# Kernel optimization log

Measured on AMD Instinct MI355X. Metric: run time of the kernel, lower is better.

Reference implementation:

```python
import jax, jax.numpy as jnp
import numpy as np
import math

D_MODEL = 1024
N_HEAD = 16          # sub-heads per branch
N_BR = 4             # hardcoded n_branches
DH = D_MODEL // N_HEAD
H_TOT = N_BR * N_HEAD
B, T = 1, 1024
SCALE = math.pi / math.sqrt(3.0)
ATTNSCALE = DH ** -0.5


def _rope(x):
    # x: [B, H, T, D]; matches torch RoPE: even/odd split, concat halves
    t_len, d = x.shape[2], x.shape[-1]
    inv_freq = 1.0 / (10000.0 ** (jnp.arange(0, d, 2, dtype=jnp.float32) / d))
    freqs = jnp.arange(t_len, dtype=jnp.float32)[:, None] * inv_freq[None, :]  # [T, D/2]
    cos, sin = jnp.cos(freqs), jnp.sin(freqs)
    x1, x2 = x[..., 0::2], x[..., 1::2]
    return jnp.concatenate([-x2 * sin + x1 * cos, x1 * sin + x2 * cos], axis=-1)


def setup_inputs() -> dict:
    key = jax.random.key(0)
    ks = jax.random.split(key, 12)
    s = D_MODEL ** -0.5
    return {
        "X": jax.random.normal(ks[0], (B, T, D_MODEL), jnp.float32),
        "W_Q": jax.random.normal(ks[1], (D_MODEL, D_MODEL * N_BR), jnp.float32) * s,
        "b_Q": jax.random.normal(ks[2], (D_MODEL * N_BR,), jnp.float32) * 0.02,
        "W_K": jax.random.normal(ks[3], (D_MODEL, D_MODEL), jnp.float32) * s,
        "b_K": jax.random.normal(ks[4], (D_MODEL,), jnp.float32) * 0.02,
        "W_V": jax.random.normal(ks[5], (D_MODEL, D_MODEL), jnp.float32) * s,
        "b_V": jax.random.normal(ks[6], (D_MODEL,), jnp.float32) * 0.02,
        "sink_scalars": jax.random.uniform(ks[7], (H_TOT,), jnp.float32, 0.0, 0.1),
        "v_nulls": jax.random.normal(ks[8], (N_BR, D_MODEL), jnp.float32) * 0.02,
        "W_O": jax.random.normal(ks[9], (N_BR, D_MODEL, D_MODEL), jnp.float32) * s,
        "W_O_bias": jax.random.normal(ks[10], (N_BR, D_MODEL), jnp.float32) * 0.02,
    }


def reference(X, W_Q, b_Q, W_K, b_K, W_V, b_V, sink_scalars, v_nulls, W_O, W_O_bias):
    Bv, Tv, C = X.shape
    # projections -> [B, H, T, Dh]
    q = (X @ W_Q + b_Q).reshape(Bv, Tv, H_TOT, DH).transpose(0, 2, 1, 3)
    k_base = (X @ W_K + b_K).reshape(Bv, Tv, N_HEAD, DH).transpose(0, 2, 1, 3)
    v_base = (X @ W_V + b_V).reshape(Bv, Tv, N_HEAD, DH).transpose(0, 2, 1, 3)
    k = jnp.tile(k_base, (1, N_BR, 1, 1))
    v = jnp.tile(v_base, (1, N_BR, 1, 1))
    q, k = _rope(q), _rope(k)

    scores = jnp.einsum("bhtd,bhsd->bhts", q, k) * ATTNSCALE
    key_self = jnp.clip(jnp.sum(k * k, axis=-1), 1e-6, None)      # [B,H,S]
    w = jax.nn.softplus(scores / jnp.sqrt(key_self)[:, :, None, :])
    causal = jnp.tril(jnp.ones((Tv, Tv), bool))                    # [T,S]
    w = jnp.where(causal, w, 0.0)
    w = w * jax.nn.sigmoid(SCALE * w)
    sinks = sink_scalars.reshape(1, H_TOT, 1, 1)
    w = jnp.where(w < sinks, 0.0, w)
    # concat-with-sink renormalization, expressed without the concat
    total = jnp.sum(w, axis=-1, keepdims=True) + sinks + 1e-6      # [B,H,T,1]
    probs_tokens = w / total
    probs_sink = sinks / total                                     # [B,H,T,1]

    out = jnp.einsum("bhts,bhsd->bhtd", probs_tokens, v)
    v_null = v_nulls.reshape(H_TOT, DH)[None, :, None, :]          # [1,H,1,Dh]
    out = out + probs_sink * v_null

    context = out.reshape(Bv, N_BR, N_HEAD, Tv, DH).transpose(0, 1, 3, 2, 4)
    context = context.reshape(Bv, N_BR, Tv, C)
    y = jnp.einsum("bntc,ncd->bntd", context, W_O) + W_O_bias[None, :, None, :]
    return y.mean(axis=1)
```

## Files before the change

### kernel.cpp

```cpp
#include <hip/hip_runtime.h>
#include <math.h>

typedef __attribute__((ext_vector_type(4))) float  f32x4;
typedef __attribute__((ext_vector_type(8))) short  bf16x8;
typedef __attribute__((ext_vector_type(4))) short  s16x4;

#define D_MODEL 1024
#define T_LEN   1024
#define H_TOT   64
#define N_HEAD  16
#define DH      64
#define SQUISH_SCALE 1.8137993642342178f

__device__ __forceinline__ float b2f(short u) {
    union { float f; unsigned b; } v; v.b = ((unsigned)(unsigned short)u) << 16; return v.f;
}
__device__ __forceinline__ short f2b(float f) {
    union { float f; unsigned b; } v; v.f = f;
    unsigned r = (v.b + 0x7FFFu + ((v.b >> 16) & 1u)) >> 16;
    return (short)r;
}
__device__ __forceinline__ unsigned cvt_pk_bf16(float lo, float hi) {
    unsigned r;
    asm("v_cvt_pk_bf16_f32 %0, %1, %2" : "=v"(r) : "v"(lo), "v"(hi));
    return r;
}
__device__ __forceinline__ void gll16(const void* g, void* l) {
    __builtin_amdgcn_global_load_lds((const __attribute__((address_space(1))) void*)g,
                                     (__attribute__((address_space(3))) void*)l, 16, 0, 0);
}

__global__ void convert_x_kernel(const float* __restrict__ src, short* __restrict__ dst) {
    int i = (blockIdx.x * 256 + threadIdx.x) * 4;
    f32x4 v = *(const f32x4*)(src + i);
    s16x4 o;
    o.x = f2b(v.x); o.y = f2b(v.y); o.z = f2b(v.z); o.w = f2b(v.w);
    *(s16x4*)(dst + i) = o;
}

__global__ __launch_bounds__(256) void transpose_convert_kernel(
    const float* __restrict__ src, int R, int C, short* __restrict__ dst, float scale) {
    __shared__ float tile[64][65];
    int c0 = blockIdx.x * 64, r0 = blockIdx.y * 64;
    int tid = threadIdx.x;
    #pragma unroll
    for (int it = 0; it < 16; ++it) {
        int lin = it * 256 + tid;
        int r = lin >> 6, c = lin & 63;
        tile[r][c] = src[(size_t)(r0 + r) * C + c0 + c];
    }
    __syncthreads();
    #pragma unroll
    for (int it = 0; it < 16; ++it) {
        int lin = it * 256 + tid;
        int cc = lin >> 6, rr = lin & 63;
        dst[(size_t)(c0 + cc) * R + r0 + rr] = f2b(tile[rr][cc] * scale);
    }
}

__global__ void bias_setup_kernel(const float* __restrict__ bQ, const float* __restrict__ bK,
                                  const float* __restrict__ bV, const float* __restrict__ bO,
                                  float* __restrict__ biasQKV, float* __restrict__ bias_mean) {
    int i = blockIdx.x * 256 + threadIdx.x;
    if (i < 4096)      biasQKV[i] = bQ[i];
    else if (i < 5120) biasQKV[i] = bK[i - 4096];
    else if (i < 6144) biasQKV[i] = bV[i - 5120];
    else if (i < 7168) {
        int c = i - 6144;
        bias_mean[c] = 0.25f * (bO[c] + bO[1024 + c] + bO[2048 + c] + bO[3072 + c]);
    }
}

__global__ void init_out_kernel(const float* __restrict__ bias_mean, float* __restrict__ out) {
    int i = (blockIdx.x * 256 + threadIdx.x) * 4;
    f32x4 v;
    v.x = bias_mean[(i)     & 1023];
    v.y = bias_mean[(i + 1) & 1023];
    v.z = bias_mean[(i + 2) & 1023];
    v.w = bias_mean[(i + 3) & 1023];
    *(f32x4*)(out + i) = v;
}

__global__ __launch_bounds__(256) void gemm_bt_kernel(
    const short* __restrict__ A, const short* __restrict__ BT,
    const float* __restrict__ bias, short* __restrict__ outB,
    int M, int N, int K) {
    __shared__ short lA[128][64];
    __shared__ short lB[128][64];
    const int tid = threadIdx.x;
    const int lane = tid & 63, wave = tid >> 6;
    const int l15 = lane & 15, l4 = lane >> 4;
    const int wr = wave >> 1, wc = wave & 1;
    const int n0 = blockIdx.x * 128, m0 = blockIdx.y * 128;

    f32x4 acc[4][4];
    const f32x4 fz = {0.f, 0.f, 0.f, 0.f};
    #pragma unroll
    for (int m = 0; m < 4; ++m)
        #pragma unroll
        for (int n = 0; n < 4; ++n) acc[m][n] = fz;

    for (int k0 = 0; k0 < K; k0 += 64) {
        __syncthreads();
        #pragma unroll
        for (int it = 0; it < 4; ++it) {
            int lin0 = it * 256 + wave * 64;
            int lin = lin0 + lane;
            int r = lin >> 3, c = (lin & 7) ^ (r & 7);
            gll16(A  + (size_t)(m0 + r) * K + k0 + c * 8, (char*)lA + lin0 * 16);
            gll16(BT + (size_t)(n0 + r) * K + k0 + c * 8, (char*)lB + lin0 * 16);
        }
        __syncthreads();
        #pragma unroll
        for (int kk = 0; kk < 2; ++kk) {
            bf16x8 af[4], bf_[4];
            #pragma unroll
            for (int m = 0; m < 4; ++m) {
                int row = wr * 64 + m * 16 + l15;
                int ch = (kk * 4 + l4) ^ (row & 7);
                af[m] = *(const bf16x8*)&lA[row][ch << 3];
            }
            #pragma unroll
            for (int n = 0; n < 4; ++n) {
                int row = wc * 64 + n * 16 + l15;
                int ch = (kk * 4 + l4) ^ (row & 7);
                bf_[n] = *(const bf16x8*)&lB[row][ch << 3];
            }
            #pragma unroll
            for (int m = 0; m < 4; ++m)
                #pragma unroll
                for (int n = 0; n < 4; ++n)
                    acc[m][n] = __builtin_amdgcn_mfma_f32_16x16x32_bf16(af[m], bf_[n], acc[m][n], 0, 0, 0);
        }
    }
    #pragma unroll
    for (int m = 0; m < 4; ++m)
        #pragma unroll
        for (int n = 0; n < 4; ++n)
            #pragma unroll
            for (int r = 0; r < 4; ++r) {
                int row = m0 + wr * 64 + m * 16 + l4 * 4 + r;
                int col = n0 + wc * 64 + n * 16 + l15;
                outB[(size_t)row * N + col] = f2b(acc[m][n][r] + bias[col]);
            }
}

__global__ __launch_bounds__(256) void gemm_bt64_splitk_kernel(
    const short* __restrict__ A, const short* __restrict__ BT,
    float* __restrict__ out, int M, int N, int K, int KSLICE) {
    __shared__ short lA[64][64];
    __shared__ short lB[64][64];
    const int tid = threadIdx.x;
    const int lane = tid & 63, wave = tid >> 6;
    const int l15 = lane & 15, l4 = lane >> 4;
    const int wr = wave >> 1, wc = wave & 1;
    const int n0 = blockIdx.x * 64, m0 = blockIdx.y * 64;
    const int kbeg = blockIdx.z * KSLICE, kend = kbeg + KSLICE;

    f32x4 acc[2][2];
    const f32x4 fz = {0.f, 0.f, 0.f, 0.f};
    #pragma unroll
    for (int m = 0; m < 2; ++m)
        #pragma unroll
        for (int n = 0; n < 2; ++n) acc[m][n] = fz;

    for (int k0 = kbeg; k0 < kend; k0 += 64) {
        __syncthreads();
        #pragma unroll
        for (int it = 0; it < 2; ++it) {
            int lin0 = it * 256 + wave * 64;
            int lin = lin0 + lane;
            int r = lin >> 3, c = (lin & 7) ^ (r & 7);
            gll16(A  + (size_t)(m0 + r) * K + k0 + c * 8, (char*)lA + lin0 * 16);
            gll16(BT + (size_t)(n0 + r) * K + k0 + c * 8, (char*)lB + lin0 * 16);
        }
        __syncthreads();
        #pragma unroll
        for (int kk = 0; kk < 2; ++kk) {
            bf16x8 af[2], bf_[2];
            #pragma unroll
            for (int m = 0; m < 2; ++m) {
                int row = wr * 32 + m * 16 + l15;
                int ch = (kk * 4 + l4) ^ (row & 7);
                af[m] = *(const bf16x8*)&lA[row][ch << 3];
            }
            #pragma unroll
            for (int n = 0; n < 2; ++n) {
                int row = wc * 32 + n * 16 + l15;
                int ch = (kk * 4 + l4) ^ (row & 7);
                bf_[n] = *(const bf16x8*)&lB[row][ch << 3];
            }
            #pragma unroll
            for (int m = 0; m < 2; ++m)
                #pragma unroll
                for (int n = 0; n < 2; ++n)
                    acc[m][n] = __builtin_amdgcn_mfma_f32_16x16x32_bf16(af[m], bf_[n], acc[m][n], 0, 0, 0);
        }
    }
    #pragma unroll
    for (int m = 0; m < 2; ++m)
        #pragma unroll
        for (int n = 0; n < 2; ++n)
            #pragma unroll
            for (int r = 0; r < 4; ++r) {
                int row = m0 + wr * 32 + m * 16 + l4 * 4 + r;
                int col = n0 + wc * 32 + n * 16 + l15;
                unsafeAtomicAdd(&out[(size_t)row * N + col], acc[m][n][r]);
            }
}

__global__ __launch_bounds__(128) void rope_qk_kernel(short* __restrict__ QKVb, float* __restrict__ ksr) {
    int t = blockIdx.x;
    int hl = threadIdx.x >> 5;
    int j  = threadIdx.x & 31;
    int head = blockIdx.y * 4 + hl;
    short* p;
    if (head < 64) p = QKVb + (size_t)t * 6144 + head * 64;
    else           p = QKVb + (size_t)t * 6144 + 4096 + (head - 64) * 64;
    float x1 = b2f(p[2 * j]), x2 = b2f(p[2 * j + 1]);
    float freq = (float)t * __builtin_exp2f(-(float)j * 0.41524101186092033f);
    float sn = __sinf(freq), cs = __cosf(freq);
    float o1 = x1 * cs - x2 * sn;
    float o2 = x1 * sn + x2 * cs;
    p[j]      = f2b(o1);
    p[32 + j] = f2b(o2);
    if (head >= 64) {
        float ss = o1 * o1 + o2 * o2;
        #pragma unroll
        for (int off = 16; off; off >>= 1) ss += __shfl_xor(ss, off, 32);
        if (j == 0) ksr[(head - 64) * 1024 + t] = 0.125f * rsqrtf(fmaxf(ss, 1e-6f));
    }
}

__global__ __launch_bounds__(256) void v_transpose_kernel(const short* __restrict__ QKVb, short* __restrict__ Vtb) {
    __shared__ short tile[64][72];
    int h = blockIdx.x, t0 = blockIdx.y * 64;
    int tid = threadIdx.x;
    #pragma unroll
    for (int it = 0; it < 16; ++it) {
        int lin = it * 256 + tid;
        int r = lin >> 6, d = lin & 63;
        tile[r][d] = QKVb[(size_t)(t0 + r) * 6144 + 5120 + h * 64 + d];
    }
    __syncthreads();
    #pragma unroll
    for (int it = 0; it < 16; ++it) {
        int lin = it * 256 + tid;
        int d = lin >> 6, c = lin & 63;
        Vtb[(size_t)(h * 64 + d) * 1024 + t0 + c] = tile[c][d];
    }
}

__global__ __launch_bounds__(256, 4) void attn_kernel(
    const short* __restrict__ QKVb, const short* __restrict__ Vtb,
    const float* __restrict__ ksr, const float* __restrict__ sinks,
    const float* __restrict__ vnulls, short* __restrict__ Ob) {
    __shared__ short lK[64][64];
    __shared__ short lV[64][64];
    __shared__ float lks[64];
    __shared__ float lvn[64];
    __shared__ short lP[4][16][64];

    const int tid = threadIdx.x;
    const int lane = tid & 63, wave = tid >> 6;
    const int l15 = lane & 15, l4 = lane >> 4;
    const int h = blockIdx.x;
    const int qt = 15 - blockIdx.y;
    const int h16 = h & 15;
    const int t0 = qt * 64;
    const float sink = sinks[h];
    if (tid < 64) lvn[tid] = vnulls[h * 64 + tid];

    const int q_abs = t0 + wave * 16 + l15;
    bf16x8 aq[2];
    #pragma unroll
    for (int kk = 0; kk < 2; ++kk)
        aq[kk] = *(const bf16x8*)(QKVb + (size_t)q_abs * 6144 + h * 64 + kk * 32 + l4 * 8);

    const f32x4 fz = {0.f, 0.f, 0.f, 0.f};
    f32x4 acc_o[4];
    #pragma unroll
    for (int n = 0; n < 4; ++n) acc_o[n] = fz;
    float tot = 0.f;

    const int nkt = qt + 1;
    for (int kt = 0; kt < nkt; ++kt) {
        int s0 = kt * 64;
        __syncthreads();
        #pragma unroll
        for (int it = 0; it < 2; ++it) {
            int lin0 = it * 256 + wave * 64;
            int lin = lin0 + lane;
            int r = lin >> 3, c = (lin & 7) ^ (r & 7);
            gll16(QKVb + (size_t)(s0 + r) * 6144 + 4096 + h16 * 64 + c * 8, (char*)lK + lin0 * 16);
            gll16(Vtb + (size_t)(h16 * 64 + r) * 1024 + s0 + c * 8,          (char*)lV + lin0 * 16);
        }
        if (tid < 64) lks[tid] = ksr[h16 * 1024 + s0 + tid];
        __syncthreads();

        f32x4 accs[4];
        #pragma unroll
        for (int n = 0; n < 4; ++n) accs[n] = fz;
        #pragma unroll
        for (int kk = 0; kk < 2; ++kk) {
            bf16x8 bk[4];
            #pragma unroll
            for (int n = 0; n < 4; ++n) {
                int row = n * 16 + l15;
                int ch = (kk * 4 + l4) ^ (row & 7);
                bk[n] = *(const bf16x8*)&lK[row][ch << 3];
            }
            #pragma unroll
            for (int n = 0; n < 4; ++n)
                accs[n] = __builtin_amdgcn_mfma_f32_16x16x32_bf16(bk[n], aq[kk], accs[n], 0, 0, 0);
        }

        #pragma unroll
        for (int n = 0; n < 4; ++n) {
            f32x4 ksv = *(const f32x4*)&lks[n * 16 + l4 * 4];
            float w4[4];
            #pragma unroll
            for (int r = 0; r < 4; ++r) {
                int k_abs = s0 + n * 16 + l4 * 4 + r;
                float z = accs[n][r] * ksv[r];
                float e = __expf(-fabsf(z));
                float w = fmaxf(z, 0.f) + __logf(1.f + e);
                w = (k_abs <= q_abs) ? w : 0.f;
                float g = __expf(-SQUISH_SCALE * w);
                w = w * __builtin_amdgcn_rcpf(1.f + g);
                w = (w >= sink) ? w : 0.f;
                tot += w;
                w4[r] = w;
            }
            unsigned pa = cvt_pk_bf16(w4[0], w4[1]);
            unsigned pb = cvt_pk_bf16(w4[2], w4[3]);
            int ch = (2 * n + (l4 >> 1)) ^ (l15 & 7);
            uint2 val; val.x = pa; val.y = pb;
            *(uint2*)&lP[wave][l15][ch * 8 + (l4 & 1) * 4] = val;
        }

        #pragma unroll
        for (int kk = 0; kk < 2; ++kk) {
            bf16x8 ap = *(const bf16x8*)&lP[wave][l15][((kk * 4 + l4) ^ (l15 & 7)) << 3];
            bf16x8 bv[4];
            #pragma unroll
            for (int n = 0; n < 4; ++n) {
                int row = n * 16 + l15;
                int ch = (kk * 4 + l4) ^ (row & 7);
                bv[n] = *(const bf16x8*)&lV[row][ch << 3];
            }
            #pragma unroll
            for (int n = 0; n < 4; ++n)
                acc_o[n] = __builtin_amdgcn_mfma_f32_16x16x32_bf16(ap, bv[n], acc_o[n], 0, 0, 0);
        }
    }

    tot += __shfl_xor(tot, 16, 64);
    tot += __shfl_xor(tot, 32, 64);
    float tq[4];
    #pragma unroll
    for (int r = 0; r < 4; ++r) tq[r] = __shfl(tot, l4 * 4 + r, 64);

    #pragma unroll
    for (int r = 0; r < 4; ++r) {
        float inv = __builtin_amdgcn_rcpf(tq[r] + sink + 1e-6f);
        int trow = t0 + wave * 16 + l4 * 4 + r;
        #pragma unroll
        for (int n = 0; n < 4; ++n) {
            int d = n * 16 + l15;
            float val = (acc_o[n][r] + sink * lvn[d]) * inv;
            Ob[(size_t)trow * 4096 + h * 64 + d] = f2b(val);
        }
    }
}

extern "C" void kernel_launch(void* const* d_in, const int* in_sizes, int n_in,
                              void* d_out, int out_size, void* d_ws, size_t ws_size,
                              hipStream_t stream) {
    const float* X        = (const float*)d_in[0];
    const float* W_Q      = (const float*)d_in[1];
    const float* b_Q      = (const float*)d_in[2];
    const float* W_K      = (const float*)d_in[3];
    const float* b_K      = (const float*)d_in[4];
    const float* W_V      = (const float*)d_in[5];
    const float* b_V      = (const float*)d_in[6];
    const float* sinks    = (const float*)d_in[7];
    const float* v_nulls  = (const float*)d_in[8];
    const float* W_O      = (const float*)d_in[9];
    const float* W_O_bias = (const float*)d_in[10];
    float* out = (float*)d_out;
    char* ws = (char*)d_ws;

    short* Xb        = (short*)(ws + 0);
    short* WbT       = (short*)(ws + 2097152);
    short* WoT       = (short*)(ws + 14680064);
    short* QKVb      = (short*)(ws + 23068672);
    short* Vtb       = (short*)(ws + 35651584);
    short* Ob        = (short*)(ws + 37748736);
    float* ksr       = (float*)(ws + 46137344);
    float* biasQKV   = (float*)(ws + 46202880);
    float* bias_mean = (float*)(ws + 46227456);

    convert_x_kernel<<<1024, 256, 0, stream>>>(X, Xb);
    transpose_convert_kernel<<<dim3(64, 16), 256, 0, stream>>>(W_Q, 1024, 4096, WbT, 1.f);
    transpose_convert_kernel<<<dim3(16, 16), 256, 0, stream>>>(W_K, 1024, 1024, WbT + 4096 * 1024, 1.f);
    transpose_convert_kernel<<<dim3(16, 16), 256, 0, stream>>>(W_V, 1024, 1024, WbT + 5120 * 1024, 1.f);
    transpose_convert_kernel<<<dim3(16, 64), 256, 0, stream>>>(W_O, 4096, 1024, WoT, 0.25f);
    bias_setup_kernel<<<28, 256, 0, stream>>>(b_Q, b_K, b_V, W_O_bias, biasQKV, bias_mean);

    gemm_bt_kernel<<<dim3(48, 8), 256, 0, stream>>>(Xb, WbT, biasQKV, QKVb, 1024, 6144, 1024);
    rope_qk_kernel<<<dim3(1024, 20), 128, 0, stream>>>(QKVb, ksr);
    v_transpose_kernel<<<dim3(16, 16), 256, 0, stream>>>(QKVb, Vtb);
    attn_kernel<<<dim3(64, 16), 256, 0, stream>>>(QKVb, Vtb, ksr, sinks, v_nulls, Ob);

    init_out_kernel<<<1024, 256, 0, stream>>>(bias_mean, out);
    gemm_bt64_splitk_kernel<<<dim3(16, 16, 4), 256, 0, stream>>>(Ob, WoT, out, 1024, 1024, 4096, 1024);
}
```

Measured before the change: 217.4 us.

## Fuse prep kernels, double-buffer GEMM and attention loads, retile split-K

Merges the X conversion, the weight transpose-converts, the bias setup and the output init into one prep kernel with vectorized loads and stores. It also merges RoPE and the V transpose into one launch. Both GEMMs and the attention kernel now double-buffer their LDS tiles, issuing the next tile's global-to-LDS loads before computing the current one, with explicit waitcnt and barriers. The output-projection split-K GEMM moves to 128x128 tiles with 8 K-slices, and attention occupancy drops to 3 blocks per SM. The goal is fewer launches and hidden load latency, paid for with more LDS use and lower occupancy.

After: 207.9 us. 1.05x faster.

```diff
diff --git a/kernel.cpp b/kernel.cpp
--- a/kernel.cpp
+++ b/kernel.cpp
@@ -5,11 +5,6 @@
 typedef __attribute__((ext_vector_type(8))) short  bf16x8;
 typedef __attribute__((ext_vector_type(4))) short  s16x4;
 
-#define D_MODEL 1024
-#define T_LEN   1024
-#define H_TOT   64
-#define N_HEAD  16
-#define DH      64
 #define SQUISH_SCALE 1.8137993642342178f
 
 __device__ __forceinline__ float b2f(short u) {
@@ -29,64 +24,87 @@
     __builtin_amdgcn_global_load_lds((const __attribute__((address_space(1))) void*)g,
                                      (__attribute__((address_space(3))) void*)l, 16, 0, 0);
 }
-
-__global__ void convert_x_kernel(const float* __restrict__ src, short* __restrict__ dst) {
-    int i = (blockIdx.x * 256 + threadIdx.x) * 4;
-    f32x4 v = *(const f32x4*)(src + i);
-    s16x4 o;
-    o.x = f2b(v.x); o.y = f2b(v.y); o.z = f2b(v.z); o.w = f2b(v.w);
-    *(s16x4*)(dst + i) = o;
-}
-
-__global__ __launch_bounds__(256) void transpose_convert_kernel(
-    const float* __restrict__ src, int R, int C, short* __restrict__ dst, float scale) {
+__device__ __forceinline__ void gll4(const void* g, void* l) {
+    __builtin_amdgcn_global_load_lds((const __attribute__((address_space(1))) void*)g,
+                                     (__attribute__((address_space(3))) void*)l, 4, 0, 0);
+}
+
+__device__ __forceinline__ void do_transpose(const float* __restrict__ src, int R, int C,
+                                             short* __restrict__ dst, float scale,
+                                             int c0, int r0, float (*tile)[65], int tid) {
+    #pragma unroll
+    for (int it = 0; it < 4; ++it) {
+        int lin = it * 256 + tid;
+        int r = lin >> 4, c4 = lin & 15;
+        f32x4 v = *(const f32x4*)(src + (size_t)(r0 + r) * C + c0 + c4 * 4);
+        #pragma unroll
+        for (int k = 0; k < 4; ++k) tile[r][c4 * 4 + k] = v[k];
+    }
+    __syncthreads();
+    #pragma unroll
+    for (int it = 0; it < 4; ++it) {
+        int lin = it * 256 + tid;
+        int c = lin >> 4, rq = lin & 15;
+        s16x4 o;
+        #pragma unroll
+        for (int k = 0; k < 4; ++k) o[k] = f2b(tile[rq * 4 + k][c] * scale);
+        *(s16x4*)(dst + (size_t)(c0 + c) * R + r0 + rq * 4) = o;
+    }
+}
+
+__global__ __launch_bounds__(256) void prep_kernel(
+    const float* __restrict__ X, const float* __restrict__ W_Q, const float* __restrict__ W_K,
+    const float* __restrict__ W_V, const float* __restrict__ W_O,
+    const float* __restrict__ bQ, const float* __restrict__ bK, const float* __restrict__ bV,
+    const float* __restrict__ bO,
+    short* __restrict__ Xb, short* __restrict__ WbT, short* __restrict__ WoT,
+    float* __restrict__ biasQKV, float* __restrict__ out) {
     __shared__ float tile[64][65];
-    int c0 = blockIdx.x * 64, r0 = blockIdx.y * 64;
-    int tid = threadIdx.x;
-    #pragma unroll
-    for (int it = 0; it < 16; ++it) {
-        int lin = it * 256 + tid;
-        int r = lin >> 6, c = lin & 63;
-        tile[r][c] = src[(size_t)(r0 + r) * C + c0 + c];
-    }
-    __syncthreads();
-    #pragma unroll
-    for (int it = 0; it < 16; ++it) {
-        int lin = it * 256 + tid;
-        int cc = lin >> 6, rr = lin & 63;
-        dst[(size_t)(c0 + cc) * R + r0 + rr] = f2b(tile[rr][cc] * scale);
-    }
-}
-
-__global__ void bias_setup_kernel(const float* __restrict__ bQ, const float* __restrict__ bK,
-                                  const float* __restrict__ bV, const float* __restrict__ bO,
-                                  float* __restrict__ biasQKV, float* __restrict__ bias_mean) {
-    int i = blockIdx.x * 256 + threadIdx.x;
-    if (i < 4096)      biasQKV[i] = bQ[i];
-    else if (i < 5120) biasQKV[i] = bK[i - 4096];
-    else if (i < 6144) biasQKV[i] = bV[i - 5120];
-    else if (i < 7168) {
-        int c = i - 6144;
-        bias_mean[c] = 0.25f * (bO[c] + bO[1024 + c] + bO[2048 + c] + bO[3072 + c]);
-    }
-}
-
-__global__ void init_out_kernel(const float* __restrict__ bias_mean, float* __restrict__ out) {
-    int i = (blockIdx.x * 256 + threadIdx.x) * 4;
-    f32x4 v;
-    v.x = bias_mean[(i)     & 1023];
-    v.y = bias_mean[(i + 1) & 1023];
-    v.z = bias_mean[(i + 2) & 1023];
-    v.w = bias_mean[(i + 3) & 1023];
-    *(f32x4*)(out + i) = v;
+    const int bid = blockIdx.x, tid = threadIdx.x;
+    if (bid < 256) {
+        int i = (bid * 256 + tid) * 16;
+        #pragma unroll
+        for (int k = 0; k < 4; ++k) {
+            f32x4 v = *(const f32x4*)(X + i + k * 4);
+            s16x4 o;
+            o.x = f2b(v.x); o.y = f2b(v.y); o.z = f2b(v.z); o.w = f2b(v.w);
+            *(s16x4*)(Xb + i + k * 4) = o;
+        }
+    } else if (bid < 1280) {
+        int b2 = bid - 256;
+        do_transpose(W_Q, 1024, 4096, WbT, 1.f, (b2 & 63) * 64, (b2 >> 6) * 64, tile, tid);
+    } else if (bid < 1536) {
+        int b2 = bid - 1280;
+        do_transpose(W_K, 1024, 1024, WbT + 4096 * 1024, 1.f, (b2 & 15) * 64, (b2 >> 4) * 64, tile, tid);
+    } else if (bid < 1792) {
+        int b2 = bid - 1536;
+        do_transpose(W_V, 1024, 1024, WbT + 5120 * 1024, 1.f, (b2 & 15) * 64, (b2 >> 4) * 64, tile, tid);
+    } else if (bid < 2816) {
+        int b2 = bid - 1792;
+        do_transpose(W_O, 4096, 1024, WoT, 0.25f, (b2 & 15) * 64, (b2 >> 4) * 64, tile, tid);
+    } else if (bid < 2840) {
+        int i = (bid - 2816) * 256 + tid;
+        if (i < 4096)      biasQKV[i] = bQ[i];
+        else if (i < 5120) biasQKV[i] = bK[i - 4096];
+        else               biasQKV[i] = bV[i - 5120];
+    } else {
+        int i = ((bid - 2840) * 256 + tid) * 4;
+        f32x4 v;
+        #pragma unroll
+        for (int k = 0; k < 4; ++k) {
+            int c = (i + k) & 1023;
+            v[k] = 0.25f * (bO[c] + bO[1024 + c] + bO[2048 + c] + bO[3072 + c]);
+        }
+        *(f32x4*)(out + i) = v;
+    }
 }
 
 __global__ __launch_bounds__(256) void gemm_bt_kernel(
     const short* __restrict__ A, const short* __restrict__ BT,
     const float* __restrict__ bias, short* __restrict__ outB,
     int M, int N, int K) {
-    __shared__ short lA[128][64];
-    __shared__ short lB[128][64];
+    __shared__ short lA[2][128][64];
+    __shared__ short lB[2][128][64];
     const int tid = threadIdx.x;
     const int lane = tid & 63, wave = tid >> 6;
     const int l15 = lane & 15, l4 = lane >> 4;
@@ -100,17 +118,26 @@
         #pragma unroll
         for (int n = 0; n < 4; ++n) acc[m][n] = fz;
 
+#define GSTAGE(k0_, b_) do {                                                   \
+    _Pragma("unroll")                                                          \
+    for (int it = 0; it < 4; ++it) {                                           \
+        int lin0 = it * 256 + wave * 64;                                       \
+        int lin = lin0 + lane;                                                 \
+        int r = lin >> 3, c = (lin & 7) ^ (r & 7);                             \
+        gll16(A  + (size_t)(m0 + r) * K + (k0_) + c * 8, (char*)lA[b_] + lin0 * 16); \
+        gll16(BT + (size_t)(n0 + r) * K + (k0_) + c * 8, (char*)lB[b_] + lin0 * 16); \
+    } } while (0)
+
+    GSTAGE(0, 0);
+    int cur = 0;
     for (int k0 = 0; k0 < K; k0 += 64) {
-        __syncthreads();
-        #pragma unroll
-        for (int it = 0; it < 4; ++it) {
-            int lin0 = it * 256 + wave * 64;
-            int lin = lin0 + lane;
-            int r = lin >> 3, c = (lin & 7) ^ (r & 7);
-            gll16(A  + (size_t)(m0 + r) * K + k0 + c * 8, (char*)lA + lin0 * 16);
-            gll16(BT + (size_t)(n0 + r) * K + k0 + c * 8, (char*)lB + lin0 * 16);
-        }
-        __syncthreads();
+        if (k0 + 64 < K) {
+            GSTAGE(k0 + 64, cur ^ 1);
+            asm volatile("s_waitcnt vmcnt(8) lgkmcnt(0)" ::: "memory");
+        } else {
+            asm volatile("s_waitcnt vmcnt(0) lgkmcnt(0)" ::: "memory");
+        }
+        __builtin_amdgcn_s_barrier();
         #pragma unroll
         for (int kk = 0; kk < 2; ++kk) {
             bf16x8 af[4], bf_[4];
@@ -118,13 +145,13 @@
             for (int m = 0; m < 4; ++m) {
                 int row = wr * 64 + m * 16 + l15;
                 int ch = (kk * 4 + l4) ^ (row & 7);
-                af[m] = *(const bf16x8*)&lA[row][ch << 3];
+                af[m] = *(const bf16x8*)&lA[cur][row][ch << 3];
             }
             #pragma unroll
             for (int n = 0; n < 4; ++n) {
                 int row = wc * 64 + n * 16 + l15;
                 int ch = (kk * 4 + l4) ^ (row & 7);
-                bf_[n] = *(const bf16x8*)&lB[row][ch << 3];
+                bf_[n] = *(const bf16x8*)&lB[cur][row][ch << 3];
             }
             #pragma unroll
             for (int m = 0; m < 4; ++m)
@@ -132,7 +159,11 @@
                 for (int n = 0; n < 4; ++n)
                     acc[m][n] = __builtin_amdgcn_mfma_f32_16x16x32_bf16(af[m], bf_[n], acc[m][n], 0, 0, 0);
         }
-    }
+        asm volatile("" ::: "memory");
+        __builtin_amdgcn_s_barrier();
+        cur ^= 1;
+    }
+#undef GSTAGE
     #pragma unroll
     for (int m = 0; m < 4; ++m)
         #pragma unroll
@@ -145,119 +176,140 @@
             }
 }
 
-__global__ __launch_bounds__(256) void gemm_bt64_splitk_kernel(
+__global__ __launch_bounds__(256) void gemm_bt_splitk_kernel(
     const short* __restrict__ A, const short* __restrict__ BT,
     float* __restrict__ out, int M, int N, int K, int KSLICE) {
-    __shared__ short lA[64][64];
-    __shared__ short lB[64][64];
+    __shared__ short lA[2][128][64];
+    __shared__ short lB[2][128][64];
     const int tid = threadIdx.x;
     const int lane = tid & 63, wave = tid >> 6;
     const int l15 = lane & 15, l4 = lane >> 4;
     const int wr = wave >> 1, wc = wave & 1;
-    const int n0 = blockIdx.x * 64, m0 = blockIdx.y * 64;
+    const int n0 = blockIdx.x * 128, m0 = blockIdx.y * 128;
     const int kbeg = blockIdx.z * KSLICE, kend = kbeg + KSLICE;
 
-    f32x4 acc[2][2];
+    f32x4 acc[4][4];
     const f32x4 fz = {0.f, 0.f, 0.f, 0.f};
     #pragma unroll
-    for (int m = 0; m < 2; ++m)
-        #pragma unroll
-        for (int n = 0; n < 2; ++n) acc[m][n] = fz;
-
+    for (int m = 0; m < 4; ++m)
+        #pragma unroll
+        for (int n = 0; n < 4; ++n) acc[m][n] = fz;
+
+#define GSTAGE(k0_, b_) do {                                                   \
+    _Pragma("unroll")                                                          \
+    for (int it = 0; it < 4; ++it) {                                           \
+        int lin0 = it * 256 + wave * 64;                                       \
+        int lin = lin0 + lane;                                                 \
+        int r = lin >> 3, c = (lin & 7) ^ (r & 7);                             \
+        gll16(A  + (size_t)(m0 + r) * K + (k0_) + c * 8, (char*)lA[b_] + lin0 * 16); \
+        gll16(BT + (size_t)(n0 + r) * K + (k0_) + c * 8, (char*)lB[b_] + lin0 * 16); \
+    } } while (0)
+
+    GSTAGE(kbeg, 0);
+    int cur = 0;
     for (int k0 = kbeg; k0 < kend; k0 += 64) {
+        if (k0 + 64 < kend) {
+            GSTAGE(k0 + 64, cur ^ 1);
+            asm volatile("s_waitcnt vmcnt(8) lgkmcnt(0)" ::: "memory");
+        } else {
+            asm volatile("s_waitcnt vmcnt(0) lgkmcnt(0)" ::: "memory");
+        }
+        __builtin_amdgcn_s_barrier();
+        #pragma unroll
+        for (int kk = 0; kk < 2; ++kk) {
+            bf16x8 af[4], bf_[4];
+            #pragma unroll
+            for (int m = 0; m < 4; ++m) {
+                int row = wr * 64 + m * 16 + l15;
+                int ch = (kk * 4 + l4) ^ (row & 7);
+                af[m] = *(const bf16x8*)&lA[cur][row][ch << 3];
+            }
+            #pragma unroll
+            for (int n = 0; n < 4; ++n) {
+                int row = wc * 64 + n * 16 + l15;
+                int ch = (kk * 4 + l4) ^ (row & 7);
+                bf_[n] = *(const bf16x8*)&lB[cur][row][ch << 3];
+            }
+            #pragma unroll
+            for (int m = 0; m < 4; ++m)
+                #pragma unroll
+                for (int n = 0; n < 4; ++n)
+                    acc[m][n] = __builtin_amdgcn_mfma_f32_16x16x32_bf16(af[m], bf_[n], acc[m][n], 0, 0, 0);
+        }
+        asm volatile("" ::: "memory");
+        __builtin_amdgcn_s_barrier();
+        cur ^= 1;
+    }
+#undef GSTAGE
+    #pragma unroll
+    for (int m = 0; m < 4; ++m)
+        #pragma unroll
+        for (int n = 0; n < 4; ++n)
+            #pragma unroll
+            for (int r = 0; r < 4; ++r) {
+                int row = m0 + wr * 64 + m * 16 + l4 * 4 + r;
+                int col = n0 + wc * 64 + n * 16 + l15;
+                unsafeAtomicAdd(&out[(size_t)row * N + col], acc[m][n][r]);
+            }
+}
+
+__global__ __launch_bounds__(256) void rope_vt_kernel(short* __restrict__ QKVb,
+                                                      float* __restrict__ ksr,
+                                                      short* __restrict__ Vtb) {
+    __shared__ short tile[64][72];
+    const int bid = blockIdx.x, tid = threadIdx.x;
+    if (bid < 1280) {
+        int base = bid * 256 + tid;
+        #pragma unroll
+        for (int it = 0; it < 8; ++it) {
+            int item = base + it * 327680;
+            int j = item & 31;
+            int rem = item >> 5;
+            int head = rem % 80;
+            int t = rem / 80;
+            short* p;
+            if (head < 64) p = QKVb + (size_t)t * 6144 + head * 64;
+            else           p = QKVb + (size_t)t * 6144 + 4096 + (head - 64) * 64;
+            float x1 = b2f(p[2 * j]), x2 = b2f(p[2 * j + 1]);
+            float freq = (float)t * __builtin_exp2f(-(float)j * 0.41524101186092033f);
+            float sn = __sinf(freq), cs = __cosf(freq);
+            float o1 = x1 * cs - x2 * sn;
+            float o2 = x1 * sn + x2 * cs;
+            p[j]      = f2b(o1);
+            p[32 + j] = f2b(o2);
+            if (head >= 64) {
+                float ss = o1 * o1 + o2 * o2;
+                #pragma unroll
+                for (int off = 16; off; off >>= 1) ss += __shfl_xor(ss, off, 32);
+                if (j == 0) ksr[(head - 64) * 1024 + t] = 0.125f * rsqrtf(fmaxf(ss, 1e-6f));
+            }
+        }
+    } else {
+        int b2 = bid - 1280;
+        int h = b2 >> 4, t0 = (b2 & 15) * 64;
+        #pragma unroll
+        for (int it = 0; it < 16; ++it) {
+            int lin = it * 256 + tid;
+            int r = lin >> 6, d = lin & 63;
+            tile[r][d] = QKVb[(size_t)(t0 + r) * 6144 + 5120 + h * 64 + d];
+        }
         __syncthreads();
         #pragma unroll
-        for (int it = 0; it < 2; ++it) {
-            int lin0 = it * 256 + wave * 64;
-            int lin = lin0 + lane;
-            int r = lin >> 3, c = (lin & 7) ^ (r & 7);
-            gll16(A  + (size_t)(m0 + r) * K + k0 + c * 8, (char*)lA + lin0 * 16);
-            gll16(BT + (size_t)(n0 + r) * K + k0 + c * 8, (char*)lB + lin0 * 16);
-        }
-        __syncthreads();
-        #pragma unroll
-        for (int kk = 0; kk < 2; ++kk) {
-            bf16x8 af[2], bf_[2];
-            #pragma unroll
-            for (int m = 0; m < 2; ++m) {
-                int row = wr * 32 + m * 16 + l15;
-                int ch = (kk * 4 + l4) ^ (row & 7);
-                af[m] = *(const bf16x8*)&lA[row][ch << 3];
-            }
-            #pragma unroll
-            for (int n = 0; n < 2; ++n) {
-                int row = wc * 32 + n * 16 + l15;
-                int ch = (kk * 4 + l4) ^ (row & 7);
-                bf_[n] = *(const bf16x8*)&lB[row][ch << 3];
-            }
-            #pragma unroll
-            for (int m = 0; m < 2; ++m)
-                #pragma unroll
-                for (int n = 0; n < 2; ++n)
-                    acc[m][n] = __builtin_amdgcn_mfma_f32_16x16x32_bf16(af[m], bf_[n], acc[m][n], 0, 0, 0);
-        }
-    }
-    #pragma unroll
-    for (int m = 0; m < 2; ++m)
-        #pragma unroll
-        for (int n = 0; n < 2; ++n)
-            #pragma unroll
-            for (int r = 0; r < 4; ++r) {
-                int row = m0 + wr * 32 + m * 16 + l4 * 4 + r;
-                int col = n0 + wc * 32 + n * 16 + l15;
-                unsafeAtomicAdd(&out[(size_t)row * N + col], acc[m][n][r]);
-            }
-}
-
-__global__ __launch_bounds__(128) void rope_qk_kernel(short* __restrict__ QKVb, float* __restrict__ ksr) {
-    int t = blockIdx.x;
-    int hl = threadIdx.x >> 5;
-    int j  = threadIdx.x & 31;
-    int head = blockIdx.y * 4 + hl;
-    short* p;
-    if (head < 64) p = QKVb + (size_t)t * 6144 + head * 64;
-    else           p = QKVb + (size_t)t * 6144 + 4096 + (head - 64) * 64;
-    float x1 = b2f(p[2 * j]), x2 = b2f(p[2 * j + 1]);
-    float freq = (float)t * __builtin_exp2f(-(float)j * 0.41524101186092033f);
-    float sn = __sinf(freq), cs = __cosf(freq);
-    float o1 = x1 * cs - x2 * sn;
-    float o2 = x1 * sn + x2 * cs;
-    p[j]      = f2b(o1);
-    p[32 + j] = f2b(o2);
-    if (head >= 64) {
-        float ss = o1 * o1 + o2 * o2;
-        #pragma unroll
-        for (int off = 16; off; off >>= 1) ss += __shfl_xor(ss, off, 32);
-        if (j == 0) ksr[(head - 64) * 1024 + t] = 0.125f * rsqrtf(fmaxf(ss, 1e-6f));
-    }
-}
-
-__global__ __launch_bounds__(256) void v_transpose_kernel(const short* __restrict__ QKVb, short* __restrict__ Vtb) {
-    __shared__ short tile[64][72];
-    int h = blockIdx.x, t0 = blockIdx.y * 64;
-    int tid = threadIdx.x;
-    #pragma unroll
-    for (int it = 0; it < 16; ++it) {
-        int lin = it * 256 + tid;
-        int r = lin >> 6, d = lin & 63;
-        tile[r][d] = QKVb[(size_t)(t0 + r) * 6144 + 5120 + h * 64 + d];
-    }
-    __syncthreads();
-    #pragma unroll
-    for (int it = 0; it < 16; ++it) {
-        int lin = it * 256 + tid;
-        int d = lin >> 6, c = lin & 63;
-        Vtb[(size_t)(h * 64 + d) * 1024 + t0 + c] = tile[c][d];
-    }
-}
-
-__global__ __launch_bounds__(256, 4) void attn_kernel(
+        for (int it = 0; it < 16; ++it) {
+            int lin = it * 256 + tid;
+            int d = lin >> 6, c = lin & 63;
+            Vtb[(size_t)(h * 64 + d) * 1024 + t0 + c] = tile[c][d];
+        }
+    }
+}
+
+__global__ __launch_bounds__(256, 3) void attn_kernel(
     const short* __restrict__ QKVb, const short* __restrict__ Vtb,
     const float* __restrict__ ksr, const float* __restrict__ sinks,
     const float* __restrict__ vnulls, short* __restrict__ Ob) {
-    __shared__ short lK[64][64];
-    __shared__ short lV[64][64];
-    __shared__ float lks[64];
+    __shared__ short lK[2][64][64];
+    __shared__ short lV[2][64][64];
+    __shared__ float lks[2][64];
     __shared__ float lvn[64];
     __shared__ short lP[4][16][64];
 
@@ -283,20 +335,30 @@
     for (int n = 0; n < 4; ++n) acc_o[n] = fz;
     float tot = 0.f;
 
+#define ASTAGE(s0_, b_) do {                                                          \
+    int lin0 = wave * 64;                                                             \
+    int lin = lin0 + lane;                                                            \
+    int r = lin >> 3, c = (lin & 7) ^ (r & 7);                                        \
+    gll16(QKVb + (size_t)((s0_) + r) * 6144 + 4096 + h16 * 64 + c * 8, (char*)lK[b_] + lin0 * 16); \
+    gll16(Vtb + (size_t)(h16 * 64 + r) * 1024 + (s0_) + c * 8,         (char*)lV[b_] + lin0 * 16); \
+    lin0 += 256; lin = lin0 + lane; r = lin >> 3; c = (lin & 7) ^ (r & 7);            \
+    gll16(QKVb + (size_t)((s0_) + r) * 6144 + 4096 + h16 * 64 + c * 8, (char*)lK[b_] + lin0 * 16); \
+    gll16(Vtb + (size_t)(h16 * 64 + r) * 1024 + (s0_) + c * 8,         (char*)lV[b_] + lin0 * 16); \
+    gll4(ksr + h16 * 1024 + (s0_) + lane, (char*)lks[b_]);                            \
+} while (0)
+
     const int nkt = qt + 1;
+    ASTAGE(0, 0);
+    int cur = 0;
     for (int kt = 0; kt < nkt; ++kt) {
         int s0 = kt * 64;
-        __syncthreads();
-        #pragma unroll
-        for (int it = 0; it < 2; ++it) {
-            int lin0 = it * 256 + wave * 64;
-            int lin = lin0 + lane;
-            int r = lin >> 3, c = (lin & 7) ^ (r & 7);
-            gll16(QKVb + (size_t)(s0 + r) * 6144 + 4096 + h16 * 64 + c * 8, (char*)lK + lin0 * 16);
-            gll16(Vtb + (size_t)(h16 * 64 + r) * 1024 + s0 + c * 8,          (char*)lV + lin0 * 16);
-        }
-        if (tid < 64) lks[tid] = ksr[h16 * 1024 + s0 + tid];
-        __syncthreads();
+        if (kt + 1 < nkt) {
+            ASTAGE(s0 + 64, cur ^ 1);
+            asm volatile("s_waitcnt vmcnt(5) lgkmcnt(0)" ::: "memory");
+        } else {
+            asm volatile("s_waitcnt vmcnt(0) lgkmcnt(0)" ::: "memory");
+        }
+        __builtin_amdgcn_s_barrier();
 
         f32x4 accs[4];
         #pragma unroll
@@ -308,7 +370,7 @@
             for (int n = 0; n < 4; ++n) {
                 int row = n * 16 + l15;
                 int ch = (kk * 4 + l4) ^ (row & 7);
-                bk[n] = *(const bf16x8*)&lK[row][ch << 3];
+                bk[n] = *(const bf16x8*)&lK[cur][row][ch << 3];
             }
             #pragma unroll
             for (int n = 0; n < 4; ++n)
@@ -317,7 +379,7 @@
 
         #pragma unroll
         for (int n = 0; n < 4; ++n) {
-            f32x4 ksv = *(const f32x4*)&lks[n * 16 + l4 * 4];
+            f32x4 ksv = *(const f32x4*)&lks[cur][n * 16 + l4 * 4];
             float w4[4];
             #pragma unroll
             for (int r = 0; r < 4; ++r) {
@@ -347,13 +409,17 @@
             for (int n = 0; n < 4; ++n) {
                 int row = n * 16 + l15;
                 int ch = (kk * 4 + l4) ^ (row & 7);
-                bv[n] = *(const bf16x8*)&lV[row][ch << 3];
+                bv[n] = *(const bf16x8*)&lV[cur][row][ch << 3];
             }
             #pragma unroll
             for (int n = 0; n < 4; ++n)
                 acc_o[n] = __builtin_amdgcn_mfma_f32_16x16x32_bf16(ap, bv[n], acc_o[n], 0, 0, 0);
         }
-    }
+        asm volatile("" ::: "memory");
+        __builtin_amdgcn_s_barrier();
+        cur ^= 1;
+    }
+#undef ASTAGE
 
     tot += __shfl_xor(tot, 16, 64);
     tot += __shfl_xor(tot, 32, 64);
@@ -399,20 +465,11 @@
     short* Ob        = (short*)(ws + 37748736);
     float* ksr       = (float*)(ws + 46137344);
     float* biasQKV   = (float*)(ws + 46202880);
-    float* bias_mean = (float*)(ws + 46227456);
-
-    convert_x_kernel<<<1024, 256, 0, stream>>>(X, Xb);
-    transpose_convert_kernel<<<dim3(64, 16), 256, 0, stream>>>(W_Q, 1024, 4096, WbT, 1.f);
-    transpose_convert_kernel<<<dim3(16, 16), 256, 0, stream>>>(W_K, 1024, 1024, WbT + 4096 * 1024, 1.f);
-    transpose_convert_kernel<<<dim3(16, 16), 256, 0, stream>>>(W_V, 1024, 1024, WbT + 5120 * 1024, 1.f);
-    transpose_convert_kernel<<<dim3(16, 64), 256, 0, stream>>>(W_O, 4096, 1024, WoT, 0.25f);
-    bias_setup_kernel<<<28, 256, 0, stream>>>(b_Q, b_K, b_V, W_O_bias, biasQKV, bias_mean);
-
+
+    prep_kernel<<<3864, 256, 0, stream>>>(X, W_Q, W_K, W_V, W_O, b_Q, b_K, b_V, W_O_bias,
+                                          Xb, WbT, WoT, biasQKV, out);
     gemm_bt_kernel<<<dim3(48, 8), 256, 0, stream>>>(Xb, WbT, biasQKV, QKVb, 1024, 6144, 1024);
-    rope_qk_kernel<<<dim3(1024, 20), 128, 0, stream>>>(QKVb, ksr);
-    v_transpose_kernel<<<dim3(16, 16), 256, 0, stream>>>(QKVb, Vtb);
+    rope_vt_kernel<<<1536, 256, 0, stream>>>(QKVb, ksr, Vtb);
     attn_kernel<<<dim3(64, 16), 256, 0, stream>>>(QKVb, Vtb, ksr, sinks, v_nulls, Ob);
-
-    init_out_kernel<<<1024, 256, 0, stream>>>(bias_mean, out);
-    gemm_bt64_splitk_kernel<<<dim3(16, 16, 4), 256, 0, stream>>>(Ob, WoT, out, 1024, 1024, 4096, 1024);
-}
+    gemm_bt_splitk_kernel<<<dim3(8, 8, 8), 256, 0, stream>>>(Ob, WoT, out, 1024, 1024, 4096, 512);
+}
```
